# Kernel tuning notes

Hardware: AMD Instinct MI355X
Metric: run time of the kernel (lower is better)

Reference implementation:

```python
import jax, jax.numpy as jnp
import numpy as np

H = 8          # head_num
NEG = -1e9     # mask fill value
LN_EPS = 1e-6


def setup_inputs() -> dict:
    key = jax.random.key(0)
    ks = jax.random.split(key, 12)
    B, S, D = 8, 1024, 512
    inp = {
        'q': jax.random.normal(ks[0], (B, S, D), jnp.float32),
        'k': jax.random.normal(ks[1], (B, S, D), jnp.float32),
        'v': jax.random.normal(ks[2], (B, S, D), jnp.float32),
        'query_mask': jax.random.randint(ks[3], (B, S), 0, 2, jnp.int32),
        'key_mask': jax.random.randint(ks[4], (B, S), 0, 2, jnp.int32),
        'Wq': jax.random.normal(ks[5], (D, D), jnp.float32) / np.sqrt(D),
        'bq': jax.random.normal(ks[6], (D,), jnp.float32) * 0.02,
        'Wk': jax.random.normal(ks[7], (D, D), jnp.float32) / np.sqrt(D),
        'bk': jax.random.normal(ks[8], (D,), jnp.float32) * 0.02,
        'Wv': jax.random.normal(ks[9], (D, D), jnp.float32) / np.sqrt(D),
        'bv': jax.random.normal(ks[10], (D,), jnp.float32) * 0.02,
        'gamma': jnp.ones((D,), jnp.float32),
        'beta': jnp.zeros((D,), jnp.float32),
    }
    return inp


def _to_batches(x):
    # [B,S,D] -> [B*H, S, D/H]  (batch-major head layout, as in torch code)
    B, S, D = x.shape
    return x.reshape(B, S, H, D // H).transpose(0, 2, 1, 3).reshape(B * H, S, D // H)


def _from_batches(x):
    BH, S, d = x.shape
    B = BH // H
    return x.reshape(B, H, S, d).transpose(0, 2, 1, 3).reshape(B, S, H * d)


def reference(q, k, v, query_mask, key_mask, Wq, bq, Wk, bk, Wv, bv, gamma, beta):
    # QKV linears + ReLU activation (activation=F.relu in original)
    _q = jax.nn.relu(q @ Wq.T + bq)
    _k = jax.nn.relu(k @ Wk.T + bk)
    _v = jax.nn.relu(v @ Wv.T + bv)
    _q, _k, _v = _to_batches(_q), _to_batches(_k), _to_batches(_v)  # [B*H,S,d]

    # masks tiled head-MAJOR (repeat(head_num,1) semantics): index = h*B + b
    km = jnp.tile(key_mask, (H, 1))[:, None, :]    # [B*H, 1, S_k]
    qm = jnp.tile(query_mask, (H, 1))[:, :, None]  # [B*H, S_q, 1]

    d = _q.shape[-1]
    scores = jnp.einsum('bqd,bkd->bqk', _q, _k) / jnp.sqrt(jnp.float32(d))
    scores = jnp.where(km == 0, NEG, scores)
    attn = jax.nn.softmax(scores, axis=-1)
    attn = attn * qm.astype(attn.dtype)            # multiplicative query mask
    # dropout: eval mode (rate applied only in training) -> identity
    y = jnp.einsum('bqk,bkd->bqd', attn, _v)
    y = _from_batches(y) + q                       # residual
    # LayerNorm over last dim
    mu = jnp.mean(y, axis=-1, keepdims=True)
    var = jnp.mean((y - mu) ** 2, axis=-1, keepdims=True)
    return gamma * (y - mu) / jnp.sqrt(var + LN_EPS) + beta
```

## Files before the change

kernel.cpp:

```cpp
#include <hip/hip_runtime.h>
#include <stdint.h>

constexpr int kB = 8, kH = 8, kS = 1024, kD = 512, kDH = 64;
constexpr float kNeg = -1e9f;
constexpr float kScaleLog2e = 0.125f * 1.4426950408889634f;

typedef __attribute__((ext_vector_type(8))) short bf16x8;
typedef __attribute__((ext_vector_type(4))) float f32x4;

__device__ __forceinline__ unsigned short f2bf(float f) {
  union { float f; unsigned int u; } a; a.f = f;
  return (unsigned short)((a.u + 0x7FFFu + ((a.u >> 16) & 1u)) >> 16);
}

#if __has_builtin(__builtin_amdgcn_exp2f)
#define EXP2F(x) __builtin_amdgcn_exp2f(x)
#else
#define EXP2F(x) exp2f(x)
#endif

__global__ __launch_bounds__(256)
void qkv_gemm_kernel(const float* __restrict__ xq, const float* __restrict__ xk,
                     const float* __restrict__ xv,
                     const float* __restrict__ wq, const float* __restrict__ wk,
                     const float* __restrict__ wv,
                     const float* __restrict__ bq, const float* __restrict__ bk,
                     const float* __restrict__ bv,
                     unsigned short* __restrict__ wsout)
{
  __shared__ __align__(16) unsigned short As[128][72];
  __shared__ __align__(16) unsigned short Bs[128][72];

  const int bid = blockIdx.x;
  const int xcd = bid & 7;
  const int j = bid >> 3;
  const int x = j & 3;
  const int g = (j >> 2) * 8 + xcd;
  const int z = g >> 6;
  const int y = g & 63;

  const float* X    = (z == 0) ? xq : (z == 1) ? xk : xv;
  const float* W    = (z == 0) ? wq : (z == 1) ? wk : wv;
  const float* bias = (z == 0) ? bq : (z == 1) ? bk : bv;
  unsigned short* out = wsout + (size_t)z * (kB * kS * kD);

  const int m0 = y * 128;
  const int n0 = x * 128;
  const int t = threadIdx.x;
  const int lane = t & 63;
  const int w = t >> 6;
  const int wr = w >> 1, wc = w & 1;
  const int l16 = lane & 15, lg = lane >> 4;

  f32x4 acc[4][4] = {};

  for (int kt = 0; kt < kD; kt += 64) {
    __syncthreads();
#pragma unroll
    for (int i = 0; i < 4; ++i) {
      const int c = t + 256 * i;
      const int row = c >> 3, c8 = (c & 7) * 8;
      const float* srcA = X + (size_t)(m0 + row) * kD + kt + c8;
      float4 a0 = *(const float4*)srcA;
      float4 a1 = *(const float4*)(srcA + 4);
      uint4 ua;
      ua.x = f2bf(a0.x) | ((unsigned)f2bf(a0.y) << 16);
      ua.y = f2bf(a0.z) | ((unsigned)f2bf(a0.w) << 16);
      ua.z = f2bf(a1.x) | ((unsigned)f2bf(a1.y) << 16);
      ua.w = f2bf(a1.z) | ((unsigned)f2bf(a1.w) << 16);
      *(uint4*)&As[row][c8] = ua;

      const float* srcB = W + (size_t)(n0 + row) * kD + kt + c8;
      float4 b0 = *(const float4*)srcB;
      float4 b1 = *(const float4*)(srcB + 4);
      uint4 ub;
      ub.x = f2bf(b0.x) | ((unsigned)f2bf(b0.y) << 16);
      ub.y = f2bf(b0.z) | ((unsigned)f2bf(b0.w) << 16);
      ub.z = f2bf(b1.x) | ((unsigned)f2bf(b1.y) << 16);
      ub.w = f2bf(b1.z) | ((unsigned)f2bf(b1.w) << 16);
      *(uint4*)&Bs[row][c8] = ub;
    }
    __syncthreads();

#pragma unroll
    for (int kk = 0; kk < 2; ++kk) {
      bf16x8 av[4];
#pragma unroll
      for (int mf = 0; mf < 4; ++mf)
        av[mf] = *(const bf16x8*)&As[wr * 64 + mf * 16 + l16][kk * 32 + lg * 8];
      if (z != 2) {
#pragma unroll
        for (int nf = 0; nf < 4; ++nf) {
          bf16x8 bfr = *(const bf16x8*)&Bs[wc * 64 + nf * 16 + l16][kk * 32 + lg * 8];
#pragma unroll
          for (int mf = 0; mf < 4; ++mf)
            acc[mf][nf] = __builtin_amdgcn_mfma_f32_16x16x32_bf16(av[mf], bfr, acc[mf][nf], 0, 0, 0);
        }
      } else {
#pragma unroll
        for (int nf = 0; nf < 4; ++nf) {
          bf16x8 bfr = *(const bf16x8*)&Bs[wc * 64 + nf * 16 + l16][kk * 32 + lg * 8];
#pragma unroll
          for (int mf = 0; mf < 4; ++mf)
            acc[mf][nf] = __builtin_amdgcn_mfma_f32_16x16x32_bf16(bfr, av[mf], acc[mf][nf], 0, 0, 0);
        }
      }
    }
  }

  if (z == 2) {
#pragma unroll
    for (int nf = 0; nf < 4; ++nf) {
#pragma unroll
      for (int r = 0; r < 4; ++r) {
        const int n = n0 + wc * 64 + nf * 16 + lg * 4 + r;
        const float bval = bias[n];
        const int h = n >> 6, dd = n & 63;
#pragma unroll
        for (int mf = 0; mf < 4; ++mf) {
          const int mm = m0 + wr * 64 + mf * 16 + l16;
          const int b_ = mm >> 10, s = mm & 1023;
          const int sp = (s & ~63) | (l16 * 4 + mf);
          float vv = acc[mf][nf][r] + bval;
          vv = vv > 0.f ? vv : 0.f;
          out[((size_t)((b_ * kH + h) * kDH + dd)) * kS + sp] = f2bf(vv);
        }
      }
    }
  } else {
#pragma unroll
    for (int nf = 0; nf < 4; ++nf) {
      const int n = n0 + wc * 64 + nf * 16 + l16;
      const float bval = bias[n];
      const int h = n >> 6, dd = n & 63;
#pragma unroll
      for (int mf = 0; mf < 4; ++mf) {
#pragma unroll
        for (int r = 0; r < 4; ++r) {
          const int m_ = m0 + wr * 64 + mf * 16 + lg * 4 + r;
          const int b_ = m_ >> 10, s = m_ & 1023;
          float vv = acc[mf][nf][r] + bval;
          vv = vv > 0.f ? vv : 0.f;
          out[((size_t)(b_ * kH + h) * kS + s) * kDH + dd] = f2bf(vv);
        }
      }
    }
  }
}

__global__ __launch_bounds__(256)
void attn_kernel(const unsigned short* __restrict__ ws,
                 const int* __restrict__ key_mask,
                 float* __restrict__ y)
{
  __shared__ __align__(16) unsigned short Ks[64][72];
  __shared__ __align__(16) unsigned short Vts[64][72];
  __shared__ __align__(16) unsigned short Ps[4][16][72];
  __shared__ float kmadd[64];

  const unsigned short* Qw = ws;
  const unsigned short* Kw = ws + (size_t)1 * kB * kS * kD;
  const unsigned short* Vw = ws + (size_t)2 * kB * kS * kD;

  const int bid = blockIdx.x;
  const int xcd = bid & 7;
  const int j = bid >> 3;
  const int qx = j & 15;
  const int bh = (j >> 4) * 8 + xcd;

  const int q0 = qx * 64;
  const int t = threadIdx.x;
  const int w = t >> 6, lane = t & 63;
  const int l16 = lane & 15, lg = lane >> 4;
  const int b_ = bh / kH, h = bh % kH;

  const unsigned short* Qb = Qw + ((size_t)bh * kS + q0) * kDH;
  const unsigned short* Kb = Kw + (size_t)bh * kS * kDH;
  const unsigned short* Vb = Vw + (size_t)bh * kDH * kS;
  const int* km = key_mask + (bh % kB) * kS;

  bf16x8 aq[2];
#pragma unroll
  for (int kk = 0; kk < 2; ++kk)
    aq[kk] = *(const bf16x8*)(Qb + (size_t)(w * 16 + l16) * kDH + kk * 32 + lg * 8);

  bf16x8 vone;
#pragma unroll
  for (int jj = 0; jj < 8; ++jj) vone[jj] = (short)0x3F80;

  f32x4 o[4] = {};
  f32x4 lacc = {};

  for (int kv0 = 0; kv0 < kS; kv0 += 64) {
    __syncthreads();
#pragma unroll
    for (int i = 0; i < 2; ++i) {
      const int c = t + 256 * i;
      const int row = c >> 3, c8 = (c & 7) * 8;
      *(uint4*)&Ks[row][c8]  = *(const uint4*)(Kb + (size_t)(kv0 + row) * kDH + c8);
      *(uint4*)&Vts[row][c8] = *(const uint4*)(Vb + (size_t)row * kS + kv0 + c8);
    }
    if (t < 64) kmadd[t] = km[kv0 + t] ? 0.f : kNeg;
    __syncthreads();

    f32x4 sc[4] = {};
#pragma unroll
    for (int kk = 0; kk < 2; ++kk) {
#pragma unroll
      for (int nf = 0; nf < 4; ++nf) {
        bf16x8 bfr = *(const bf16x8*)&Ks[nf * 16 + l16][kk * 32 + lg * 8];
        sc[nf] = __builtin_amdgcn_mfma_f32_16x16x32_bf16(aq[kk], bfr, sc[nf], 0, 0, 0);
      }
    }

    float madd[4];
#pragma unroll
    for (int nf = 0; nf < 4; ++nf) madd[nf] = kmadd[nf * 16 + l16];

#pragma unroll
    for (int r = 0; r < 4; ++r) {
      const float p0 = EXP2F(fmaf(sc[0][r], kScaleLog2e, madd[0]));
      const float p1 = EXP2F(fmaf(sc[1][r], kScaleLog2e, madd[1]));
      const float p2 = EXP2F(fmaf(sc[2][r], kScaleLog2e, madd[2]));
      const float p3 = EXP2F(fmaf(sc[3][r], kScaleLog2e, madd[3]));
      const int prow = lg * 4 + r;
      uint2 pw;
      pw.x = __builtin_amdgcn_perm(__float_as_uint(p1), __float_as_uint(p0), 0x07060302u);
      pw.y = __builtin_amdgcn_perm(__float_as_uint(p3), __float_as_uint(p2), 0x07060302u);
      *(uint2*)&Ps[w][prow][l16 * 4] = pw;
    }

#pragma unroll
    for (int kk = 0; kk < 2; ++kk) {
      bf16x8 a = *(const bf16x8*)&Ps[w][l16][kk * 32 + lg * 8];
#pragma unroll
      for (int nd = 0; nd < 4; ++nd) {
        bf16x8 bfr = *(const bf16x8*)&Vts[nd * 16 + l16][kk * 32 + lg * 8];
        o[nd] = __builtin_amdgcn_mfma_f32_16x16x32_bf16(a, bfr, o[nd], 0, 0, 0);
      }
      lacc = __builtin_amdgcn_mfma_f32_16x16x32_bf16(a, vone, lacc, 0, 0, 0);
    }
  }

  float rinv[4];
#pragma unroll
  for (int r = 0; r < 4; ++r) rinv[r] = 1.f / lacc[r];
#pragma unroll
  for (int nd = 0; nd < 4; ++nd) {
#pragma unroll
    for (int r = 0; r < 4; ++r) {
      const int srow = q0 + w * 16 + lg * 4 + r;
      y[((size_t)b_ * kS + srow) * kD + h * kDH + nd * 16 + l16] = o[nd][r] * rinv[r];
    }
  }
}

__global__ __launch_bounds__(256)
void ln_kernel(const float* __restrict__ y, const float* __restrict__ q,
               const int* __restrict__ qmask,
               const float* __restrict__ gamma, const float* __restrict__ beta,
               float* __restrict__ out)
{
  const int w = threadIdx.x >> 6, lane = threadIdx.x & 63;
  const int row = blockIdx.x * 4 + w;
  const int b_ = row >> 10, s = row & 1023;
  const int d0 = lane * 8;
  const int h = d0 >> 6;

  const float* yp = y + (size_t)row * kD + d0;
  const float* qp = q + (size_t)row * kD + d0;
  const int qm = qmask[((b_ * kH + h) % kB) * kS + s];

  float4 y0 = *(const float4*)yp, y1 = *(const float4*)(yp + 4);
  float4 q0 = *(const float4*)qp, q1 = *(const float4*)(qp + 4);
  float vals[8] = { y0.x, y0.y, y0.z, y0.w, y1.x, y1.y, y1.z, y1.w };
  float qs[8]   = { q0.x, q0.y, q0.z, q0.w, q1.x, q1.y, q1.z, q1.w };

  float sum = 0.f, ss = 0.f;
#pragma unroll
  for (int j = 0; j < 8; ++j) {
    const float val = (qm ? vals[j] : 0.f) + qs[j];
    vals[j] = val; sum += val; ss += val * val;
  }
#pragma unroll
  for (int off = 1; off < 64; off <<= 1) {
    sum += __shfl_xor(sum, off);
    ss  += __shfl_xor(ss, off);
  }
  const float mu = sum * (1.f / kD);
  const float var = ss * (1.f / kD) - mu * mu;
  const float rstd = rsqrtf(var + 1e-6f);

  float4 g0 = *(const float4*)(gamma + d0), g1 = *(const float4*)(gamma + d0 + 4);
  float4 be0 = *(const float4*)(beta + d0), be1 = *(const float4*)(beta + d0 + 4);
  float gs[8] = { g0.x, g0.y, g0.z, g0.w, g1.x, g1.y, g1.z, g1.w };
  float bs[8] = { be0.x, be0.y, be0.z, be0.w, be1.x, be1.y, be1.z, be1.w };

  float4 o0, o1;
  o0.x = gs[0] * (vals[0] - mu) * rstd + bs[0];
  o0.y = gs[1] * (vals[1] - mu) * rstd + bs[1];
  o0.z = gs[2] * (vals[2] - mu) * rstd + bs[2];
  o0.w = gs[3] * (vals[3] - mu) * rstd + bs[3];
  o1.x = gs[4] * (vals[4] - mu) * rstd + bs[4];
  o1.y = gs[5] * (vals[5] - mu) * rstd + bs[5];
  o1.z = gs[6] * (vals[6] - mu) * rstd + bs[6];
  o1.w = gs[7] * (vals[7] - mu) * rstd + bs[7];
  *(float4*)(out + (size_t)row * kD + d0) = o0;
  *(float4*)(out + (size_t)row * kD + d0 + 4) = o1;
}

extern "C" void kernel_launch(void* const* d_in, const int* in_sizes, int n_in,
                              void* d_out, int out_size, void* d_ws, size_t ws_size,
                              hipStream_t stream) {
  const float* q  = (const float*)d_in[0];
  const float* k  = (const float*)d_in[1];
  const float* v  = (const float*)d_in[2];
  const int* qmask = (const int*)d_in[3];
  const int* kmask = (const int*)d_in[4];
  const float* Wq = (const float*)d_in[5];
  const float* bq = (const float*)d_in[6];
  const float* Wk = (const float*)d_in[7];
  const float* bk = (const float*)d_in[8];
  const float* Wv = (const float*)d_in[9];
  const float* bv = (const float*)d_in[10];
  const float* gamma = (const float*)d_in[11];
  const float* beta  = (const float*)d_in[12];
  float* out = (float*)d_out;
  unsigned short* wsqkv = (unsigned short*)d_ws;

  qkv_gemm_kernel<<<768, 256, 0, stream>>>(
      q, k, v, Wq, Wk, Wv, bq, bk, bv, wsqkv);
  attn_kernel<<<1024, 256, 0, stream>>>(wsqkv, kmask, out);
  ln_kernel<<<2048, 256, 0, stream>>>(out, q, qmask, gamma, beta, out);
}
```

Measured before the change: 81.07 us.

## Pre-convert weights to bf16, register-prefetch GEMM tiles, use 512-thread blocks, vectorize stores

Adds a small kernel that converts the three weight matrices to bf16 once per call, staging them in the output buffer as scratch, so the GEMM no longer converts weights per tile. The QKV GEMM now uses 512 threads (8 waves, 64x32 per wave) and double-buffers the next k-tile's global loads in registers to overlap loads with MFMA work. The z==2 branch is unified by always using the swapped operand order. Epilogue stores are packed into 4-element bf16 vectors. This costs an extra kernel launch and overwrites the output buffer before attention writes it.

```diff
diff --git a/kernel.cpp b/kernel.cpp
--- a/kernel.cpp
+++ b/kernel.cpp
@@ -1,4 +1,5 @@
 #include <hip/hip_runtime.h>
+#include <hip/hip_bf16.h>
 #include <stdint.h>
 
 constexpr int kB = 8, kH = 8, kS = 1024, kD = 512, kDH = 64;
@@ -7,10 +8,17 @@
 
 typedef __attribute__((ext_vector_type(8))) short bf16x8;
 typedef __attribute__((ext_vector_type(4))) float f32x4;
+typedef __attribute__((ext_vector_type(4))) unsigned short u16x4;
 
 __device__ __forceinline__ unsigned short f2bf(float f) {
   union { float f; unsigned int u; } a; a.f = f;
   return (unsigned short)((a.u + 0x7FFFu + ((a.u >> 16) & 1u)) >> 16);
+}
+
+__device__ __forceinline__ unsigned int pk2bf(float lo, float hi) {
+  union { __hip_bfloat162 h; unsigned int u; } cv;
+  cv.h = __float22bfloat162_rn(make_float2(lo, hi));
+  return cv.u;
 }
 
 #if __has_builtin(__builtin_amdgcn_exp2f)
@@ -20,10 +28,23 @@
 #endif
 
 __global__ __launch_bounds__(256)
+void wcvt_kernel(const float* __restrict__ wq, const float* __restrict__ wk,
+                 const float* __restrict__ wv, unsigned short* __restrict__ wout)
+{
+  const int tid = blockIdx.x * 256 + threadIdx.x;
+  const int z = tid >> 16;
+  const int i = (tid & 65535) * 4;
+  const float* W = (z == 0) ? wq : (z == 1) ? wk : wv;
+  float4 v4 = *(const float4*)(W + i);
+  u16x4 pk;
+  pk[0] = f2bf(v4.x); pk[1] = f2bf(v4.y); pk[2] = f2bf(v4.z); pk[3] = f2bf(v4.w);
+  *(u16x4*)(wout + (size_t)z * 262144 + i) = pk;
+}
+
+__global__ __launch_bounds__(512, 4)
 void qkv_gemm_kernel(const float* __restrict__ xq, const float* __restrict__ xk,
                      const float* __restrict__ xv,
-                     const float* __restrict__ wq, const float* __restrict__ wk,
-                     const float* __restrict__ wv,
+                     const unsigned short* __restrict__ wbf,
                      const float* __restrict__ bq, const float* __restrict__ bk,
                      const float* __restrict__ bv,
                      unsigned short* __restrict__ wsout)
@@ -40,7 +61,7 @@
   const int y = g & 63;
 
   const float* X    = (z == 0) ? xq : (z == 1) ? xk : xv;
-  const float* W    = (z == 0) ? wq : (z == 1) ? wk : wv;
+  const unsigned short* Wb = wbf + (size_t)z * 262144;
   const float* bias = (z == 0) ? bq : (z == 1) ? bk : bv;
   unsigned short* out = wsout + (size_t)z * (kB * kS * kD);
 
@@ -49,100 +70,103 @@
   const int t = threadIdx.x;
   const int lane = t & 63;
   const int w = t >> 6;
-  const int wr = w >> 1, wc = w & 1;
+  const int wr = w >> 2, wc = w & 3;
   const int l16 = lane & 15, lg = lane >> 4;
 
-  f32x4 acc[4][4] = {};
-
-  for (int kt = 0; kt < kD; kt += 64) {
+  f32x4 acc[4][2] = {};
+  float4 pa[2][4];
+  uint4  pb[2][2];
+
+#pragma unroll
+  for (int i = 0; i < 2; ++i) {
+    const int c = t + 512 * i;
+    const int row = c >> 3, c8 = (c & 7) * 8;
+    pa[0][2 * i]     = *(const float4*)(X + (size_t)(m0 + row) * kD + c8);
+    pa[0][2 * i + 1] = *(const float4*)(X + (size_t)(m0 + row) * kD + c8 + 4);
+    pb[0][i]         = *(const uint4*)(Wb + (size_t)(n0 + row) * kD + c8);
+  }
+
+#pragma unroll
+  for (int kt8 = 0; kt8 < 8; ++kt8) {
+    const int p = kt8 & 1;
     __syncthreads();
 #pragma unroll
-    for (int i = 0; i < 4; ++i) {
-      const int c = t + 256 * i;
+    for (int i = 0; i < 2; ++i) {
+      const int c = t + 512 * i;
       const int row = c >> 3, c8 = (c & 7) * 8;
-      const float* srcA = X + (size_t)(m0 + row) * kD + kt + c8;
-      float4 a0 = *(const float4*)srcA;
-      float4 a1 = *(const float4*)(srcA + 4);
       uint4 ua;
-      ua.x = f2bf(a0.x) | ((unsigned)f2bf(a0.y) << 16);
-      ua.y = f2bf(a0.z) | ((unsigned)f2bf(a0.w) << 16);
-      ua.z = f2bf(a1.x) | ((unsigned)f2bf(a1.y) << 16);
-      ua.w = f2bf(a1.z) | ((unsigned)f2bf(a1.w) << 16);
+      ua.x = pk2bf(pa[p][2 * i].x, pa[p][2 * i].y);
+      ua.y = pk2bf(pa[p][2 * i].z, pa[p][2 * i].w);
+      ua.z = pk2bf(pa[p][2 * i + 1].x, pa[p][2 * i + 1].y);
+      ua.w = pk2bf(pa[p][2 * i + 1].z, pa[p][2 * i + 1].w);
       *(uint4*)&As[row][c8] = ua;
-
-      const float* srcB = W + (size_t)(n0 + row) * kD + kt + c8;
-      float4 b0 = *(const float4*)srcB;
-      float4 b1 = *(const float4*)(srcB + 4);
-      uint4 ub;
-      ub.x = f2bf(b0.x) | ((unsigned)f2bf(b0.y) << 16);
-      ub.y = f2bf(b0.z) | ((unsigned)f2bf(b0.w) << 16);
-      ub.z = f2bf(b1.x) | ((unsigned)f2bf(b1.y) << 16);
-      ub.w = f2bf(b1.z) | ((unsigned)f2bf(b1.w) << 16);
-      *(uint4*)&Bs[row][c8] = ub;
+      *(uint4*)&Bs[row][c8] = pb[p][i];
+    }
+    if (kt8 < 7) {
+      const int ktn = (kt8 + 1) * 64;
+#pragma unroll
+      for (int i = 0; i < 2; ++i) {
+        const int c = t + 512 * i;
+        const int row = c >> 3, c8 = (c & 7) * 8;
+        pa[p ^ 1][2 * i]     = *(const float4*)(X + (size_t)(m0 + row) * kD + ktn + c8);
+        pa[p ^ 1][2 * i + 1] = *(const float4*)(X + (size_t)(m0 + row) * kD + ktn + c8 + 4);
+        pb[p ^ 1][i]         = *(const uint4*)(Wb + (size_t)(n0 + row) * kD + ktn + c8);
+      }
     }
     __syncthreads();
-
 #pragma unroll
     for (int kk = 0; kk < 2; ++kk) {
       bf16x8 av[4];
 #pragma unroll
       for (int mf = 0; mf < 4; ++mf)
         av[mf] = *(const bf16x8*)&As[wr * 64 + mf * 16 + l16][kk * 32 + lg * 8];
-      if (z != 2) {
-#pragma unroll
-        for (int nf = 0; nf < 4; ++nf) {
-          bf16x8 bfr = *(const bf16x8*)&Bs[wc * 64 + nf * 16 + l16][kk * 32 + lg * 8];
-#pragma unroll
-          for (int mf = 0; mf < 4; ++mf)
-            acc[mf][nf] = __builtin_amdgcn_mfma_f32_16x16x32_bf16(av[mf], bfr, acc[mf][nf], 0, 0, 0);
-        }
-      } else {
-#pragma unroll
-        for (int nf = 0; nf < 4; ++nf) {
-          bf16x8 bfr = *(const bf16x8*)&Bs[wc * 64 + nf * 16 + l16][kk * 32 + lg * 8];
-#pragma unroll
-          for (int mf = 0; mf < 4; ++mf)
-            acc[mf][nf] = __builtin_amdgcn_mfma_f32_16x16x32_bf16(bfr, av[mf], acc[mf][nf], 0, 0, 0);
-        }
+#pragma unroll
+      for (int nf = 0; nf < 2; ++nf) {
+        bf16x8 bfr = *(const bf16x8*)&Bs[wc * 32 + nf * 16 + l16][kk * 32 + lg * 8];
+#pragma unroll
+        for (int mf = 0; mf < 4; ++mf)
+          acc[mf][nf] = __builtin_amdgcn_mfma_f32_16x16x32_bf16(bfr, av[mf], acc[mf][nf], 0, 0, 0);
       }
     }
   }
 
   if (z == 2) {
-#pragma unroll
-    for (int nf = 0; nf < 4; ++nf) {
+    const int mmbase = m0 + wr * 64;
+    const int b_ = mmbase >> 10, sbase = mmbase & 1023;
+#pragma unroll
+    for (int nf = 0; nf < 2; ++nf) {
 #pragma unroll
       for (int r = 0; r < 4; ++r) {
-        const int n = n0 + wc * 64 + nf * 16 + lg * 4 + r;
+        const int n = n0 + wc * 32 + nf * 16 + lg * 4 + r;
         const float bval = bias[n];
         const int h = n >> 6, dd = n & 63;
+        u16x4 pk;
 #pragma unroll
         for (int mf = 0; mf < 4; ++mf) {
-          const int mm = m0 + wr * 64 + mf * 16 + l16;
-          const int b_ = mm >> 10, s = mm & 1023;
-          const int sp = (s & ~63) | (l16 * 4 + mf);
           float vv = acc[mf][nf][r] + bval;
           vv = vv > 0.f ? vv : 0.f;
-          out[((size_t)((b_ * kH + h) * kDH + dd)) * kS + sp] = f2bf(vv);
+          pk[mf] = f2bf(vv);
         }
+        *(u16x4*)&out[((size_t)((b_ * kH + h) * kDH + dd)) * kS + sbase + l16 * 4] = pk;
       }
     }
   } else {
 #pragma unroll
-    for (int nf = 0; nf < 4; ++nf) {
-      const int n = n0 + wc * 64 + nf * 16 + l16;
-      const float bval = bias[n];
-      const int h = n >> 6, dd = n & 63;
-#pragma unroll
-      for (int mf = 0; mf < 4; ++mf) {
+    for (int mf = 0; mf < 4; ++mf) {
+      const int mm = m0 + wr * 64 + mf * 16 + l16;
+      const int b_ = mm >> 10, s = mm & 1023;
+#pragma unroll
+      for (int nf = 0; nf < 2; ++nf) {
+        const int nbase = n0 + wc * 32 + nf * 16 + lg * 4;
+        const int h = nbase >> 6, dd = nbase & 63;
+        u16x4 pk;
 #pragma unroll
         for (int r = 0; r < 4; ++r) {
-          const int m_ = m0 + wr * 64 + mf * 16 + lg * 4 + r;
-          const int b_ = m_ >> 10, s = m_ & 1023;
-          float vv = acc[mf][nf][r] + bval;
+          float vv = acc[mf][nf][r] + bias[nbase + r];
           vv = vv > 0.f ? vv : 0.f;
-          out[((size_t)(b_ * kH + h) * kS + s) * kDH + dd] = f2bf(vv);
+          pk[r] = f2bf(vv);
         }
+        *(u16x4*)&out[((size_t)(b_ * kH + h) * kS + s) * kDH + dd] = pk;
       }
     }
   }
@@ -327,9 +351,11 @@
   const float* beta  = (const float*)d_in[12];
   float* out = (float*)d_out;
   unsigned short* wsqkv = (unsigned short*)d_ws;
-
-  qkv_gemm_kernel<<<768, 256, 0, stream>>>(
-      q, k, v, Wq, Wk, Wv, bq, bk, bv, wsqkv);
+  unsigned short* wbf = (unsigned short*)d_out;
+
+  wcvt_kernel<<<768, 256, 0, stream>>>(Wq, Wk, Wv, wbf);
+  qkv_gemm_kernel<<<768, 512, 0, stream>>>(
+      q, k, v, wbf, bq, bk, bv, wsqkv);
   attn_kernel<<<1024, 256, 0, stream>>>(wsqkv, kmask, out);
   ln_kernel<<<2048, 256, 0, stream>>>(out, q, qmask, gamma, beta, out);
 }
```

Measured after the change: 98.28 us. 1.21x slower.
